# Kernel tuning notes

Hardware: AMD Instinct MI355X
Metric: run time of the kernel (lower is better)

## Reference

```python
import jax, jax.numpy as jnp
import numpy as np

T, B, D = 1024, 64, 256   # time, batch, input dim
L, DC = 1024, 256         # context length, context dim
H, A = 256, 256           # hidden, attention dim
NEG = -1e9


def setup_inputs() -> dict:
    key = jax.random.key(0)
    ks = jax.random.split(key, 12)
    s = lambda fan: 1.0 / np.sqrt(fan)
    inp = {
        'x': jax.random.normal(ks[0], (T, B, D), jnp.float32),
        'lengths': jnp.maximum(jax.random.randint(ks[1], (B,), 1, T + 1), 1).astype(jnp.int32),
        'context': jax.random.normal(ks[2], (B, L, DC), jnp.float32),
        'ctx_lengths': jnp.maximum(jax.random.randint(ks[3], (B,), 1, L + 1), 1).astype(jnp.int32),
        'Wc': jax.random.normal(ks[4], (DC, A), jnp.float32) * s(DC),
        'Wx': jax.random.normal(ks[5], (D, A), jnp.float32) * s(D),
        'Wh': jax.random.normal(ks[6], (H, A), jnp.float32) * s(H),
        'v': jax.random.normal(ks[7], (A,), jnp.float32) * s(A),
        'W_ih': jax.random.normal(ks[8], (D + DC, 3 * H), jnp.float32) * s(D + DC),
        'W_hh': jax.random.normal(ks[9], (H, 3 * H), jnp.float32) * s(H),
        'b_ih': jnp.zeros((3 * H,), jnp.float32),
        'b_hh': jnp.zeros((3 * H,), jnp.float32),
    }
    return inp


def reference(x, lengths, context, ctx_lengths, Wc, Wx, Wh, v, W_ih, W_hh, b_ih, b_hh):
    # Precompute context projection once (shared across all timesteps). [B, L, A]
    ctx_proj = jnp.einsum('bld,da->bla', context, Wc)
    ctx_mask = jnp.arange(L)[None, :] < ctx_lengths[:, None]  # [B, L]
    h0 = jnp.zeros((B, H), x.dtype)

    def step(h, inputs):
        xt, t = inputs  # xt: [B, D]
        # Additive attention over the context.
        e = jnp.tanh(ctx_proj + (xt @ Wx)[:, None, :] + (h @ Wh)[:, None, :])  # [B, L, A]
        scores = jnp.where(ctx_mask, jnp.einsum('bla,a->bl', e, v), NEG)
        alpha = jax.nn.softmax(scores, axis=-1)                  # [B, L]
        c = jnp.einsum('bl,bld->bd', alpha, context)             # [B, DC]
        # GRU over [x_t ; c_t].
        z = jnp.concatenate([xt, c], axis=-1)                    # [B, D+DC]
        gi = z @ W_ih + b_ih
        gh = h @ W_hh + b_hh
        r = jax.nn.sigmoid(gi[:, :H] + gh[:, :H])
        u = jax.nn.sigmoid(gi[:, H:2 * H] + gh[:, H:2 * H])
        n = jnp.tanh(gi[:, 2 * H:] + r * gh[:, 2 * H:])
        h_new = u * h + (1.0 - u) * n
        valid = (t < lengths)[:, None]                           # ragged masking
        h_next = jnp.where(valid, h_new, h)
        out = jnp.where(valid, h_new, 0.0)
        return h_next, out

    h_final, outputs = jax.lax.scan(step, h0, (x, jnp.arange(T)))
    return outputs, h_final[None]  # [T, B, H], [num_layers=1, B, H]
```

## Files before the change

### kernel.cpp

```cpp
#include <hip/hip_runtime.h>
#include <cstddef>

#define T_ 1024
#define B_ 64
#define D_ 256
#define L_ 1024
#define DC_ 256
#define H_ 256
#define A_ 256
#define G3 768
#define LQ 256
#define NBLK 4

typedef unsigned int uint2v __attribute__((ext_vector_type(2)));
typedef float float4v __attribute__((ext_vector_type(4)));

__device__ __forceinline__ float bflo(unsigned int w) { return __uint_as_float(w << 16); }
__device__ __forceinline__ float bfhi(unsigned int w) { return __uint_as_float(w & 0xffff0000u); }
__device__ __forceinline__ unsigned short f2bf(float f) {
  unsigned int x = __float_as_uint(f);
  return (unsigned short)((x + 0x7fffu + ((x >> 16) & 1u)) >> 16);
}
__device__ __forceinline__ float fast_tanh(float xx) {
  float e = __expf(2.0f * xx);
  return 1.0f - 2.0f / (e + 1.0f);
}
__device__ __forceinline__ float sigmoidf_(float xx) {
  return 1.0f / (1.0f + __expf(-xx));
}
__device__ __forceinline__ void st_agent_f(float* p, float v) {
  __hip_atomic_store(p, v, __ATOMIC_RELAXED, __HIP_MEMORY_SCOPE_AGENT);
}
__device__ __forceinline__ float ld_agent_f(const float* p) {
  return __hip_atomic_load(p, __ATOMIC_RELAXED, __HIP_MEMORY_SCOPE_AGENT);
}
__device__ __forceinline__ void group_sync(unsigned int* ctrb, unsigned int target) {
  __syncthreads();
  if (threadIdx.x == 0) {
    __hip_atomic_fetch_add(ctrb, 1u, __ATOMIC_RELEASE, __HIP_MEMORY_SCOPE_AGENT);
    while (__hip_atomic_load(ctrb, __ATOMIC_ACQUIRE, __HIP_MEMORY_SCOPE_AGENT) < target) {
      __builtin_amdgcn_s_sleep(2);
    }
  }
  __syncthreads();
}

__global__ void f2bf_kernel(const float* __restrict__ src,
                            unsigned short* __restrict__ dst, int n) {
  int i = (blockIdx.x * blockDim.x + threadIdx.x) * 4;
  if (i < n) {
    float4 v = *(const float4*)(src + i);
    ushort4 o;
    o.x = f2bf(v.x); o.y = f2bf(v.y); o.z = f2bf(v.z); o.w = f2bf(v.w);
    *(ushort4*)(dst + i) = o;
  }
}

__global__ void pack_wih_kernel(const float* __restrict__ W_ih,
                                unsigned short* __restrict__ dst) {
  int idx = blockIdx.x * 256 + threadIdx.x;
  int kb = idx / (512 * 192);
  int rem = idx % (512 * 192);
  int r = rem / 192, jg = rem % 192;
  int g = jg >> 6, jj = jg & 63;
  int j = g * 256 + kb * 64 + jj;
  dst[idx] = f2bf(W_ih[(size_t)r * G3 + j]);
}
__global__ void pack_whh_kernel(const float* __restrict__ W_hh,
                                unsigned short* __restrict__ dst) {
  int idx = blockIdx.x * 256 + threadIdx.x;
  int kb = idx / (256 * 192);
  int rem = idx % (256 * 192);
  int r = rem / 192, jg = rem % 192;
  int g = jg >> 6, jj = jg & 63;
  int j = g * 256 + kb * 64 + jj;
  dst[idx] = f2bf(W_hh[(size_t)r * G3 + j]);
}

__global__ void ctx_proj_kernel(const float* __restrict__ context,
                                const float* __restrict__ Wc,
                                unsigned short* __restrict__ ctxT) {
  __shared__ float cs[4352];
  const int bid = blockIdx.x;
  const int b = bid >> 6;
  const int l0 = (bid & 63) << 4;
  const int tid = threadIdx.x;
  for (int idx = tid; idx < 16 * DC_; idx += 256) {
    int r = idx >> 8;
    int d = idx & 255;
    cs[r * DC_ + d] = context[((size_t)b * L_ + (l0 + r)) * DC_ + d];
  }
  __syncthreads();
  const int a = tid;
  float acc[16];
#pragma unroll
  for (int r = 0; r < 16; ++r) acc[r] = 0.0f;
  for (int d = 0; d < DC_; ++d) {
    float w = Wc[d * A_ + a];
#pragma unroll
    for (int r = 0; r < 16; ++r) acc[r] += cs[r * DC_ + d] * w;
  }
  __syncthreads();
#pragma unroll
  for (int r = 0; r < 16; ++r) cs[a * 17 + r] = acc[r];
  __syncthreads();
  for (int idx = tid; idx < 16 * A_; idx += 256) {
    int aa = idx >> 4;
    int r = idx & 15;
    ctxT[((size_t)b * A_ + aa) * L_ + l0 + r] = f2bf(cs[aa * 17 + r]);
  }
}

__global__ __launch_bounds__(1024) void encoder_kernel(
    const float* __restrict__ x, const int* __restrict__ lengths,
    const float* __restrict__ context, const int* __restrict__ ctx_lengths,
    const unsigned short* __restrict__ wx_b, const unsigned short* __restrict__ wh_b,
    const float* __restrict__ v,
    const unsigned short* __restrict__ wih_pk, const unsigned short* __restrict__ whh_pk,
    const float* __restrict__ b_ih, const float* __restrict__ b_hh,
    const unsigned short* __restrict__ ctxT, float* __restrict__ out,
    float* __restrict__ cpart, float* __restrict__ hx, unsigned int* __restrict__ ctr) {
  __shared__ __align__(16) float xt_s[D_];
  __shared__ __align__(16) float h_s[H_];
  __shared__ __align__(16) float c_s[DC_];
  __shared__ float2 qv_s[A_];
  __shared__ __align__(16) float part[4096];
  __shared__ __align__(16) float phh[3072];
  __shared__ float pv_s[LQ];
  __shared__ float gatI[192], gatH[192];
  __shared__ float bsl_i[192], bsl_h[192];
  __shared__ float wsum_l[4];

  const int gb = blockIdx.x;
  const int b = gb >> 2, kb = gb & 3;
  const int tid = threadIdx.x;
  const int len = lengths[b];
  const int clen = ctx_lengths[b];
  const int lbase = kb * LQ;
  const unsigned short* ctxTb = ctxT + (size_t)b * A_ * L_;
  const float* ctxb = context + (size_t)b * L_ * DC_;
  const unsigned short* wihp = wih_pk + (size_t)kb * (512 * 192);
  const unsigned short* whhp = whh_pk + (size_t)kb * (256 * 192);
  float* cpart_grp = cpart + (size_t)b * NBLK * 264;
  float* cpart_my = cpart_grp + kb * 264;
  float* hx_b = hx + (size_t)b * 256;
  unsigned int* ctr_b = ctr + b * 32;

  const int p16 = tid >> 6, i64 = tid & 63;

  if (tid < 256) { h_s[tid] = 0.0f; qv_s[tid] = make_float2(0.0f, v[tid]); }
  if (tid < 192) {
    int g = tid >> 6, jj = tid & 63;
    int j = g * 256 + kb * 64 + jj;
    bsl_i[tid] = b_ih[j]; bsl_h[tid] = b_hh[j];
  }
  __syncthreads();

  for (int t = 0; t < len; ++t) {
    if (tid < 64) {
      float4v xv = __builtin_nontemporal_load(
          (const float4v*)&x[((size_t)t * B_ + b) * D_ + tid * 4]);
      *(float4v*)&xt_s[tid * 4] = xv;
    }
    __syncthreads();

    {
      const int a0 = i64 * 4, k0 = p16 * 16;
      float4v acc = {0.f, 0.f, 0.f, 0.f};
#pragma unroll
      for (int k = k0; k < k0 + 16; ++k) {
        float xv = xt_s[k];
        uint2v w = *(const uint2v*)(wx_b + (size_t)k * A_ + a0);
        acc.x += xv * bflo(w.x); acc.y += xv * bfhi(w.x);
        acc.z += xv * bflo(w.y); acc.w += xv * bfhi(w.y);
      }
#pragma unroll
      for (int k = k0; k < k0 + 16; ++k) {
        float hv = h_s[k];
        uint2v w = *(const uint2v*)(wh_b + (size_t)k * A_ + a0);
        acc.x += hv * bflo(w.x); acc.y += hv * bfhi(w.x);
        acc.z += hv * bflo(w.y); acc.w += hv * bfhi(w.y);
      }
      *(float4v*)&part[tid * 4] = acc;
    }
    __syncthreads();
    if (tid < 256) {
      float q = 0.f;
#pragma unroll
      for (int p = 0; p < 16; ++p) q += part[p * 256 + tid];
      qv_s[tid].x = q;
    }
    __syncthreads();

    {
      const int ll0 = i64 * 4;
      float4v acc = {0.f, 0.f, 0.f, 0.f};
      if (lbase + ll0 < clen) {
        const unsigned short* basep = ctxTb + (size_t)(p16 * 16) * L_ + lbase + ll0;
#pragma unroll 4
        for (int aa = 0; aa < 16; ++aa) {
          uint2v w = __builtin_nontemporal_load((const uint2v*)(basep + (size_t)aa * L_));
          float2 qv = qv_s[p16 * 16 + aa];
          acc.x += qv.y * fast_tanh(bflo(w.x) + qv.x);
          acc.y += qv.y * fast_tanh(bfhi(w.x) + qv.x);
          acc.z += qv.y * fast_tanh(bflo(w.y) + qv.x);
          acc.w += qv.y * fast_tanh(bfhi(w.y) + qv.x);
        }
      }
      *(float4v*)&part[tid * 4] = acc;
    }
    __syncthreads();
    if (tid < 256) {
      float s = 0.f;
#pragma unroll
      for (int p = 0; p < 16; ++p) s += part[p * 256 + tid];
      int lg = lbase + tid;
      float e = (lg < clen) ? __expf(s) : 0.f;
      pv_s[tid] = e;
      float sm = e;
#pragma unroll
      for (int off = 32; off; off >>= 1) sm += __shfl_xor(sm, off);
      if ((tid & 63) == 0) wsum_l[tid >> 6] = sm;
    }
    __syncthreads();

    {
      const int d0 = i64 * 4;
      const int lmax = min(LQ, max(0, clen - lbase));
      const int l0 = p16 * 16, l1 = min(l0 + 16, lmax);
      float4v acc = {0.f, 0.f, 0.f, 0.f};
      for (int l = l0; l < l1; ++l) {
        float pv = pv_s[l];
        float4v cv = __builtin_nontemporal_load(
            (const float4v*)&ctxb[(size_t)(lbase + l) * DC_ + d0]);
        acc.x += pv * cv.x; acc.y += pv * cv.y; acc.z += pv * cv.z; acc.w += pv * cv.w;
      }
      *(float4v*)&part[tid * 4] = acc;
    }
    __syncthreads();
    if (tid < 256) {
      float cp = 0.f;
#pragma unroll
      for (int p = 0; p < 16; ++p) cp += part[p * 256 + tid];
      st_agent_f(&cpart_my[tid], cp);
    }
    if (tid == 0) {
      st_agent_f(&cpart_my[256], wsum_l[0] + wsum_l[1] + wsum_l[2] + wsum_l[3]);
    }
    group_sync(ctr_b, 8u * t + 4u);
    if (tid < 256) {
      float cc = 0.f, ss = 0.f;
#pragma unroll
      for (int k2 = 0; k2 < 4; ++k2) {
        cc += ld_agent_f(cpart_grp + k2 * 264 + tid);
        ss += ld_agent_f(cpart_grp + k2 * 264 + 256);
      }
      c_s[tid] = cc / ss;
    }
    __syncthreads();

    if (tid < 768) {
      const int pq = tid / 48, jg4 = tid % 48;
      float4v ai = {0.f, 0.f, 0.f, 0.f};
      {
        const int r0 = pq * 32;
#pragma unroll 8
        for (int r = r0; r < r0 + 32; ++r) {
          float zk = (r < 256) ? xt_s[r] : c_s[r - 256];
          uint2v w = *(const uint2v*)(wihp + (size_t)r * 192 + jg4 * 4);
          ai.x += zk * bflo(w.x); ai.y += zk * bfhi(w.x);
          ai.z += zk * bflo(w.y); ai.w += zk * bfhi(w.y);
        }
      }
      float4v ah = {0.f, 0.f, 0.f, 0.f};
      {
        const int r0 = pq * 16;
#pragma unroll 8
        for (int r = r0; r < r0 + 16; ++r) {
          float hv = h_s[r];
          uint2v w = *(const uint2v*)(whhp + (size_t)r * 192 + jg4 * 4);
          ah.x += hv * bflo(w.x); ah.y += hv * bfhi(w.x);
          ah.z += hv * bflo(w.y); ah.w += hv * bfhi(w.y);
        }
      }
      *(float4v*)&part[pq * 192 + jg4 * 4] = ai;
      *(float4v*)&phh[pq * 192 + jg4 * 4] = ah;
    }
    __syncthreads();
    if (tid < 192) {
      float gi = bsl_i[tid], gh = bsl_h[tid];
#pragma unroll
      for (int p = 0; p < 16; ++p) { gi += part[p * 192 + tid]; gh += phh[p * 192 + tid]; }
      gatI[tid] = gi; gatH[tid] = gh;
    }
    __syncthreads();
    if (tid < 64) {
      float r = sigmoidf_(gatI[tid] + gatH[tid]);
      float u = sigmoidf_(gatI[64 + tid] + gatH[64 + tid]);
      float n = fast_tanh(gatI[128 + tid] + r * gatH[128 + tid]);
      float hn = u * h_s[kb * 64 + tid] + (1.0f - u) * n;
      st_agent_f(&hx_b[kb * 64 + tid], hn);
      __builtin_nontemporal_store(hn, &out[((size_t)t * B_ + b) * H_ + kb * 64 + tid]);
    }
    group_sync(ctr_b, 8u * t + 8u);
    if (tid < 256) h_s[tid] = ld_agent_f(&hx_b[tid]);
    __syncthreads();
  }

  {
    const int n = (T_ - len) * 64;
    for (int idx = tid; idx < n; idx += 1024) {
      int tt = len + (idx >> 6);
      int ii = idx & 63;
      __builtin_nontemporal_store(0.0f, &out[((size_t)tt * B_ + b) * H_ + kb * 64 + ii]);
    }
  }
  if (tid < 64) {
    out[(size_t)T_ * B_ * H_ + (size_t)b * H_ + kb * 64 + tid] = h_s[kb * 64 + tid];
  }
}

extern "C" void kernel_launch(void* const* d_in, const int* in_sizes, int n_in,
                              void* d_out, int out_size, void* d_ws, size_t ws_size,
                              hipStream_t stream) {
  const float* x = (const float*)d_in[0];
  const int* lengths = (const int*)d_in[1];
  const float* context = (const float*)d_in[2];
  const int* ctx_lengths = (const int*)d_in[3];
  const float* Wc = (const float*)d_in[4];
  const float* Wx = (const float*)d_in[5];
  const float* Wh = (const float*)d_in[6];
  const float* v = (const float*)d_in[7];
  const float* W_ih = (const float*)d_in[8];
  const float* W_hh = (const float*)d_in[9];
  const float* b_ih = (const float*)d_in[10];
  const float* b_hh = (const float*)d_in[11];
  float* out = (float*)d_out;

  char* w = (char*)d_ws;
  unsigned short* ctxT = (unsigned short*)w;
  unsigned short* wx_b = (unsigned short*)(w + 33554432);
  unsigned short* wh_b = (unsigned short*)(w + 33685504);
  unsigned short* wih_pk = (unsigned short*)(w + 33816576);
  unsigned short* whh_pk = (unsigned short*)(w + 34603008);
  float* cpart = (float*)(w + 34996224);
  float* hx = (float*)(w + 35266560);
  unsigned int* ctr = (unsigned int*)(w + 35332096);

  hipMemsetAsync(ctr, 0, 8192, stream);
  hipLaunchKernelGGL(f2bf_kernel, dim3(64), dim3(256), 0, stream, Wx, wx_b, D_ * A_);
  hipLaunchKernelGGL(f2bf_kernel, dim3(64), dim3(256), 0, stream, Wh, wh_b, H_ * A_);
  hipLaunchKernelGGL(pack_wih_kernel, dim3(1536), dim3(256), 0, stream, W_ih, wih_pk);
  hipLaunchKernelGGL(pack_whh_kernel, dim3(768), dim3(256), 0, stream, W_hh, whh_pk);
  hipLaunchKernelGGL(ctx_proj_kernel, dim3(B_ * (L_ / 16)), dim3(256), 0, stream,
                     context, Wc, ctxT);
  hipLaunchKernelGGL(encoder_kernel, dim3(B_ * NBLK), dim3(1024), 0, stream,
                     x, lengths, context, ctx_lengths, wx_b, wh_b, v,
                     wih_pk, whh_pk, b_ih, b_hh, ctxT, out, cpart, hx, ctr);
}
```

Baseline: 53.55 ms.

## Cache per-block bf16 context projection slice in LDS and re-split GRU gate matvec

Each block now loads its 256x256 bf16 slice of the transposed context projection into shared memory (128 KB) once before the time loop. The per-step attention score loop reads it from LDS instead of global memory, removing 1024 steps of repeated global or L2 traffic. The part/phh buffers are merged into one scratch array to fit LDS. The GRU gate matvec is repartitioned into 8 row-groups by 96 column-pairs with 2-wide accumulators, and the nontemporal load hints are dropped. The large LDS footprint may limit occupancy and adds a startup load.

```diff
diff --git a/kernel.cpp b/kernel.cpp
--- a/kernel.cpp
+++ b/kernel.cpp
@@ -14,6 +14,7 @@
 
 typedef unsigned int uint2v __attribute__((ext_vector_type(2)));
 typedef float float4v __attribute__((ext_vector_type(4)));
+typedef float float2v __attribute__((ext_vector_type(2)));
 
 __device__ __forceinline__ float bflo(unsigned int w) { return __uint_as_float(w << 16); }
 __device__ __forceinline__ float bfhi(unsigned int w) { return __uint_as_float(w & 0xffff0000u); }
@@ -120,12 +121,12 @@
     const float* __restrict__ b_ih, const float* __restrict__ b_hh,
     const unsigned short* __restrict__ ctxT, float* __restrict__ out,
     float* __restrict__ cpart, float* __restrict__ hx, unsigned int* __restrict__ ctr) {
+  __shared__ __align__(16) unsigned short ctx_lds[A_ * LQ];
+  __shared__ __align__(16) float scratch[4096];
   __shared__ __align__(16) float xt_s[D_];
   __shared__ __align__(16) float h_s[H_];
   __shared__ __align__(16) float c_s[DC_];
   __shared__ float2 qv_s[A_];
-  __shared__ __align__(16) float part[4096];
-  __shared__ __align__(16) float phh[3072];
   __shared__ float pv_s[LQ];
   __shared__ float gatI[192], gatH[192];
   __shared__ float bsl_i[192], bsl_h[192];
@@ -154,13 +155,18 @@
     int j = g * 256 + kb * 64 + jj;
     bsl_i[tid] = b_ih[j]; bsl_h[tid] = b_hh[j];
   }
+  for (int idx = tid; idx < 16384; idx += 1024) {
+    int a = idx >> 6;
+    int lq = idx & 63;
+    *(uint2v*)&ctx_lds[a * LQ + lq * 4] =
+        *(const uint2v*)(ctxTb + (size_t)a * L_ + lbase + lq * 4);
+  }
   __syncthreads();
 
   for (int t = 0; t < len; ++t) {
     if (tid < 64) {
-      float4v xv = __builtin_nontemporal_load(
-          (const float4v*)&x[((size_t)t * B_ + b) * D_ + tid * 4]);
-      *(float4v*)&xt_s[tid * 4] = xv;
+      *(float4v*)&xt_s[tid * 4] =
+          *(const float4v*)&x[((size_t)t * B_ + b) * D_ + tid * 4];
     }
     __syncthreads();
 
@@ -181,13 +187,13 @@
         acc.x += hv * bflo(w.x); acc.y += hv * bfhi(w.x);
         acc.z += hv * bflo(w.y); acc.w += hv * bfhi(w.y);
       }
-      *(float4v*)&part[tid * 4] = acc;
+      *(float4v*)&scratch[tid * 4] = acc;
     }
     __syncthreads();
     if (tid < 256) {
       float q = 0.f;
 #pragma unroll
-      for (int p = 0; p < 16; ++p) q += part[p * 256 + tid];
+      for (int p = 0; p < 16; ++p) q += scratch[p * 256 + tid];
       qv_s[tid].x = q;
     }
     __syncthreads();
@@ -196,10 +202,10 @@
       const int ll0 = i64 * 4;
       float4v acc = {0.f, 0.f, 0.f, 0.f};
       if (lbase + ll0 < clen) {
-        const unsigned short* basep = ctxTb + (size_t)(p16 * 16) * L_ + lbase + ll0;
+        const unsigned short* basep = ctx_lds + p16 * 16 * LQ + ll0;
 #pragma unroll 4
         for (int aa = 0; aa < 16; ++aa) {
-          uint2v w = __builtin_nontemporal_load((const uint2v*)(basep + (size_t)aa * L_));
+          uint2v w = *(const uint2v*)(basep + aa * LQ);
           float2 qv = qv_s[p16 * 16 + aa];
           acc.x += qv.y * fast_tanh(bflo(w.x) + qv.x);
           acc.y += qv.y * fast_tanh(bfhi(w.x) + qv.x);
@@ -207,13 +213,13 @@
           acc.w += qv.y * fast_tanh(bfhi(w.y) + qv.x);
         }
       }
-      *(float4v*)&part[tid * 4] = acc;
+      *(float4v*)&scratch[tid * 4] = acc;
     }
     __syncthreads();
     if (tid < 256) {
       float s = 0.f;
 #pragma unroll
-      for (int p = 0; p < 16; ++p) s += part[p * 256 + tid];
+      for (int p = 0; p < 16; ++p) s += scratch[p * 256 + tid];
       int lg = lbase + tid;
       float e = (lg < clen) ? __expf(s) : 0.f;
       pv_s[tid] = e;
@@ -231,17 +237,16 @@
       float4v acc = {0.f, 0.f, 0.f, 0.f};
       for (int l = l0; l < l1; ++l) {
         float pv = pv_s[l];
-        float4v cv = __builtin_nontemporal_load(
-            (const float4v*)&ctxb[(size_t)(lbase + l) * DC_ + d0]);
+        float4v cv = *(const float4v*)&ctxb[(size_t)(lbase + l) * DC_ + d0];
         acc.x += pv * cv.x; acc.y += pv * cv.y; acc.z += pv * cv.z; acc.w += pv * cv.w;
       }
-      *(float4v*)&part[tid * 4] = acc;
+      *(float4v*)&scratch[tid * 4] = acc;
     }
     __syncthreads();
     if (tid < 256) {
       float cp = 0.f;
 #pragma unroll
-      for (int p = 0; p < 16; ++p) cp += part[p * 256 + tid];
+      for (int p = 0; p < 16; ++p) cp += scratch[p * 256 + tid];
       st_agent_f(&cpart_my[tid], cp);
     }
     if (tid == 0) {
@@ -260,37 +265,37 @@
     __syncthreads();
 
     if (tid < 768) {
-      const int pq = tid / 48, jg4 = tid % 48;
-      float4v ai = {0.f, 0.f, 0.f, 0.f};
-      {
-        const int r0 = pq * 32;
+      const int pq = tid / 96;
+      const int jc = tid % 96;
+      const float* zsrc = (pq < 4) ? xt_s : c_s;
+      const int zoff = (pq < 4) ? pq * 64 : (pq - 4) * 64;
+      const int r0 = pq * 64;
+      float a0 = 0.f, a1 = 0.f;
 #pragma unroll 8
-        for (int r = r0; r < r0 + 32; ++r) {
-          float zk = (r < 256) ? xt_s[r] : c_s[r - 256];
-          uint2v w = *(const uint2v*)(wihp + (size_t)r * 192 + jg4 * 4);
-          ai.x += zk * bflo(w.x); ai.y += zk * bfhi(w.x);
-          ai.z += zk * bflo(w.y); ai.w += zk * bfhi(w.y);
-        }
-      }
-      float4v ah = {0.f, 0.f, 0.f, 0.f};
-      {
-        const int r0 = pq * 16;
+      for (int i = 0; i < 64; ++i) {
+        float zk = zsrc[zoff + i];
+        unsigned int w = *(const unsigned int*)(wihp + (size_t)(r0 + i) * 192 + 2 * jc);
+        a0 += zk * bflo(w); a1 += zk * bfhi(w);
+      }
+      const int rh0 = pq * 32;
+      float h0 = 0.f, h1 = 0.f;
 #pragma unroll 8
-        for (int r = r0; r < r0 + 16; ++r) {
-          float hv = h_s[r];
-          uint2v w = *(const uint2v*)(whhp + (size_t)r * 192 + jg4 * 4);
-          ah.x += hv * bflo(w.x); ah.y += hv * bfhi(w.x);
-          ah.z += hv * bflo(w.y); ah.w += hv * bfhi(w.y);
-        }
-      }
-      *(float4v*)&part[pq * 192 + jg4 * 4] = ai;
-      *(float4v*)&phh[pq * 192 + jg4 * 4] = ah;
+      for (int i = 0; i < 32; ++i) {
+        float hv = h_s[rh0 + i];
+        unsigned int w = *(const unsigned int*)(whhp + (size_t)(rh0 + i) * 192 + 2 * jc);
+        h0 += hv * bflo(w); h1 += hv * bfhi(w);
+      }
+      *(float2v*)&scratch[pq * 192 + 2 * jc] = float2v{a0, a1};
+      *(float2v*)&scratch[1536 + pq * 192 + 2 * jc] = float2v{h0, h1};
     }
     __syncthreads();
     if (tid < 192) {
       float gi = bsl_i[tid], gh = bsl_h[tid];
 #pragma unroll
-      for (int p = 0; p < 16; ++p) { gi += part[p * 192 + tid]; gh += phh[p * 192 + tid]; }
+      for (int p = 0; p < 8; ++p) {
+        gi += scratch[p * 192 + tid];
+        gh += scratch[1536 + p * 192 + tid];
+      }
       gatI[tid] = gi; gatH[tid] = gh;
     }
     __syncthreads();
```

After: 56.16 ms. 1.05x slower.
